# Kernel tuning notes

Measured on AMD Instinct MI355X. Metric: run time of the kernel, lower is better.

Reference implementation:

```python
import jax, jax.numpy as jnp
import numpy as np

MARGIN = 2.0


def setup_inputs() -> dict:
    key = jax.random.key(0)
    k1, k2 = jax.random.split(key)
    B, D, NUM_CLASSES = 8192, 128, 100
    features = jax.random.normal(k1, (B, D), dtype=jnp.float32)
    labels = jax.random.randint(k2, (B,), 0, NUM_CLASSES, dtype=jnp.int64)
    return {"features": features, "labels": labels}


def reference(features, labels):
    # Vectorized form of the O(B^2) nested-loop contrastive loss.
    B = features.shape[0]
    sq = jnp.sum(features * features, axis=-1)                      # [B]
    # squared pairwise L2 distances via the gram matrix
    d2 = sq[:, None] + sq[None, :] - 2.0 * (features @ features.T)  # [B, B]
    d2 = jnp.maximum(d2, 0.0)

    off_diag = ~jnp.eye(B, dtype=bool)
    same = labels[:, None] == labels[None, :]
    pos_mask = same & off_diag
    neg_mask = (~same) & off_diag

    # positive pairs contribute squared distance
    pos_loss = jnp.sum(jnp.where(pos_mask, d2, 0.0))

    # negative pairs contribute clamp(margin - dist, 0)^2; guard sqrt(0) grads
    d = jnp.sqrt(jnp.where(neg_mask, d2, 1.0))
    hinge = jnp.maximum(MARGIN - d, 0.0)
    neg_loss = jnp.sum(jnp.where(neg_mask, hinge * hinge, 0.0))

    pos_count = jnp.sum(pos_mask)
    total_pairs = jnp.asarray(B * (B - 1), dtype=d2.dtype)
    loss = pos_loss + neg_loss
    # original divides only when positive_pairs > 0
    return jnp.where(pos_count > 0, loss / total_pairs, loss)
```

## Files before the change

kernel.cpp:

```cpp
#include <hip/hip_runtime.h>
#include <hip/hip_bf16.h>


#define BN 8192
#define DD 128
#define NTILES 64
#define NBLOCKS (NTILES * (NTILES + 1) / 2)

typedef __attribute__((ext_vector_type(8))) short bf16x8;
typedef __attribute__((ext_vector_type(4))) float f32x4;

__global__ __launch_bounds__(256) void prep_kernel(const float* __restrict__ f,
        const int* __restrict__ labels, short* __restrict__ fbp,
        float2* __restrict__ meta) {
    const int tid = threadIdx.x;
    const int wave = tid >> 6, lane = tid & 63;
    const int p = blockIdx.x * 4 + wave;
    const int l15 = lane & 15, quad = lane >> 4;
    const int row = p * 16 + l15;

    float s = 0.f;
#pragma unroll
    for (int ks = 0; ks < 4; ks++) {
        const float* src = f + (size_t)row * DD + ks * 32 + quad * 8;
        float4 a = *(const float4*)src;
        float4 b = *(const float4*)(src + 4);
        unsigned short u[8];
        float rv[8] = {a.x, a.y, a.z, a.w, b.x, b.y, b.z, b.w};
#pragma unroll
        for (int j = 0; j < 8; j++) {
            __hip_bfloat16 h = __float2bfloat16(rv[j]);
            u[j] = *(unsigned short*)&h;
            float r = __bfloat162float(h);
            s = fmaf(r, r, s);
        }
        bf16x8 pack;
#pragma unroll
        for (int j = 0; j < 8; j++) pack[j] = (short)u[j];
        *(bf16x8*)(fbp + ((size_t)(p * 4 + ks) * 64 + lane) * 8) = pack;
    }
    s += __shfl_xor(s, 16, 64);
    s += __shfl_xor(s, 32, 64);
    if (quad == 0) meta[row] = make_float2(s, (float)labels[row]);
}

__global__ __launch_bounds__(256) void pair_kernel(
        const short* __restrict__ fbp, const float2* __restrict__ meta,
        float2* __restrict__ partial) {
    const int t = blockIdx.x;
    int by = (int)((sqrtf(8.f * (float)t + 1.f) - 1.f) * 0.5f);
    while ((by + 1) * (by + 2) / 2 <= t) by++;
    while (by * (by + 1) / 2 > t) by--;
    const int bx = t - by * (by + 1) / 2;
    const bool diag = (bx == by);

    const int tid = threadIdx.x;
    const int wave = tid >> 6, lane = tid & 63;
    const int wx = wave & 1, wy = wave >> 1;
    const int i0 = bx * 128 + wy * 64;
    const int j0 = by * 128 + wx * 64;
    const int ip = i0 >> 4, jp = j0 >> 4;
    const int l15 = lane & 15, quad = lane >> 4;

    float pos = 0.f, neg = 0.f;

    if (!(diag && wx < wy)) {
        float2 mj[4];
#pragma unroll
        for (int ni = 0; ni < 4; ni++) mj[ni] = meta[j0 + ni * 16 + l15];
        float2 mi[4][4];
#pragma unroll
        for (int m = 0; m < 4; m++)
#pragma unroll
            for (int r = 0; r < 4; r++) mi[m][r] = meta[i0 + m * 16 + quad * 4 + r];

        f32x4 acc4[4][4];
#pragma unroll
        for (int a = 0; a < 4; a++)
#pragma unroll
            for (int b = 0; b < 4; b++) acc4[a][b] = (f32x4){0.f, 0.f, 0.f, 0.f};

#pragma unroll
        for (int ks = 0; ks < 4; ks++) {
            bf16x8 af[4], bg[4];
#pragma unroll
            for (int tt = 0; tt < 4; tt++)
                af[tt] = *(const bf16x8*)(fbp +
                    ((size_t)((ip + tt) * 4 + ks) * 64 + lane) * 8);
#pragma unroll
            for (int tt = 0; tt < 4; tt++)
                bg[tt] = *(const bf16x8*)(fbp +
                    ((size_t)((jp + tt) * 4 + ks) * 64 + lane) * 8);
#pragma unroll
            for (int m = 0; m < 4; m++)
#pragma unroll
                for (int n = 0; n < 4; n++)
                    acc4[m][n] = __builtin_amdgcn_mfma_f32_16x16x32_bf16(
                        af[m], bg[n], acc4[m][n], 0, 0, 0);
        }

        const bool strict = diag && (wx == wy);
#pragma unroll
        for (int m = 0; m < 4; m++)
#pragma unroll
            for (int n = 0; n < 4; n++)
#pragma unroll
                for (int r = 0; r < 4; r++) {
                    int il = m * 16 + quad * 4 + r;
                    int jl = n * 16 + l15;
                    bool valid = !strict || (il < jl);
                    float d2 = fmaxf(mi[m][r].x + mj[n].x - 2.f * acc4[m][n][r], 0.f);
                    if (valid) {
                        if (mi[m][r].y == mj[n].y) pos += d2;
                        else if (d2 < 4.0f) {
                            float h = 2.0f - sqrtf(d2);
                            neg += h * h;
                        }
                    }
                }
    }

#pragma unroll
    for (int off = 32; off > 0; off >>= 1) {
        pos += __shfl_down(pos, off, 64);
        neg += __shfl_down(neg, off, 64);
    }
    __shared__ float red[2][4];
    if (lane == 0) { red[0][wave] = pos; red[1][wave] = neg; }
    __syncthreads();
    if (tid == 0)
        partial[t] = make_float2(red[0][0] + red[0][1] + red[0][2] + red[0][3],
                                 red[1][0] + red[1][1] + red[1][2] + red[1][3]);
}

__global__ __launch_bounds__(256) void reduce_kernel(
        const float2* __restrict__ partial, float* __restrict__ out) {
    const int tid = threadIdx.x;
    float p = 0.f, n = 0.f;
    for (int i = tid; i < NBLOCKS; i += 256) {
        float2 v = partial[i];
        p += v.x; n += v.y;
    }
#pragma unroll
    for (int off = 32; off > 0; off >>= 1) {
        p += __shfl_down(p, off, 64);
        n += __shfl_down(n, off, 64);
    }
    __shared__ float red[2][4];
    int lane = tid & 63, w = tid >> 6;
    if (lane == 0) { red[0][w] = p; red[1][w] = n; }
    __syncthreads();
    if (tid == 0) {
        float total = 2.0f * (red[0][0] + red[0][1] + red[0][2] + red[0][3] +
                              red[1][0] + red[1][1] + red[1][2] + red[1][3]);
        out[0] = total / 67100672.0f;
    }
}

extern "C" void kernel_launch(void* const* d_in, const int* in_sizes, int n_in,
                              void* d_out, int out_size, void* d_ws, size_t ws_size,
                              hipStream_t stream) {
    const float* f = (const float*)d_in[0];
    const int* labels = (const int*)d_in[1];
    float* out = (float*)d_out;

    short* fbp = (short*)d_ws;
    float2* meta = (float2*)((char*)d_ws + (size_t)BN * DD * sizeof(short));
    float2* partial = meta + BN;

    prep_kernel<<<BN / 64, 256, 0, stream>>>(f, labels, fbp, meta);
    pair_kernel<<<NBLOCKS, 256, 0, stream>>>(fbp, meta, partial);
    reduce_kernel<<<1, 256, 0, stream>>>(partial, out);
}
```

Measured before the change: 89.76 us.

## Coalesce prep loads via LDS transpose and double-buffer MFMA operand loads

The prep kernel now has each block handle 16 rows. It reads them with fully coalesced row-contiguous float4 loads, converts to bf16 into padded shared memory, and then writes the MFMA-packed layout from LDS. The old version used strided per-lane reads. The grid grows to BN/16 blocks. In the pair kernel, the k-step loop is manually software-pipelined with two register buffers so global loads for the next k-slice are issued before the current MFMAs. This hides load latency at the cost of extra VGPRs.

New measurement: 88.19 us. Within noise of the previous version (-1.8%).

```diff
diff --git a/kernel.cpp b/kernel.cpp
--- a/kernel.cpp
+++ b/kernel.cpp
@@ -6,6 +6,7 @@
 #define DD 128
 #define NTILES 64
 #define NBLOCKS (NTILES * (NTILES + 1) / 2)
+#define LS 136
 
 typedef __attribute__((ext_vector_type(8))) short bf16x8;
 typedef __attribute__((ext_vector_type(4))) float f32x4;
@@ -14,34 +15,32 @@
         const int* __restrict__ labels, short* __restrict__ fbp,
         float2* __restrict__ meta) {
     const int tid = threadIdx.x;
-    const int wave = tid >> 6, lane = tid & 63;
-    const int p = blockIdx.x * 4 + wave;
-    const int l15 = lane & 15, quad = lane >> 4;
-    const int row = p * 16 + l15;
+    const int p = blockIdx.x;
+    __shared__ unsigned short ls[16][LS];
 
+    const int r = tid >> 4;
+    const int c = (tid & 15) * 8;
+    const float* src = f + ((size_t)p * 16 + r) * DD + c;
+    float4 a = *(const float4*)src;
+    float4 b = *(const float4*)(src + 4);
+    float rv[8] = {a.x, a.y, a.z, a.w, b.x, b.y, b.z, b.w};
     float s = 0.f;
 #pragma unroll
-    for (int ks = 0; ks < 4; ks++) {
-        const float* src = f + (size_t)row * DD + ks * 32 + quad * 8;
-        float4 a = *(const float4*)src;
-        float4 b = *(const float4*)(src + 4);
-        unsigned short u[8];
-        float rv[8] = {a.x, a.y, a.z, a.w, b.x, b.y, b.z, b.w};
+    for (int j = 0; j < 8; j++) {
+        __hip_bfloat16 h = __float2bfloat16(rv[j]);
+        ls[r][c + j] = *(unsigned short*)&h;
+        float rr = __bfloat162float(h);
+        s = fmaf(rr, rr, s);
+    }
 #pragma unroll
-        for (int j = 0; j < 8; j++) {
-            __hip_bfloat16 h = __float2bfloat16(rv[j]);
-            u[j] = *(unsigned short*)&h;
-            float r = __bfloat162float(h);
-            s = fmaf(r, r, s);
-        }
-        bf16x8 pack;
-#pragma unroll
-        for (int j = 0; j < 8; j++) pack[j] = (short)u[j];
-        *(bf16x8*)(fbp + ((size_t)(p * 4 + ks) * 64 + lane) * 8) = pack;
-    }
-    s += __shfl_xor(s, 16, 64);
-    s += __shfl_xor(s, 32, 64);
-    if (quad == 0) meta[row] = make_float2(s, (float)labels[row]);
+    for (int off = 8; off > 0; off >>= 1) s += __shfl_down(s, off, 16);
+    if ((tid & 15) == 0) meta[p * 16 + r] = make_float2(s, (float)labels[p * 16 + r]);
+    __syncthreads();
+
+    const int w = tid >> 6, lane = tid & 63;
+    const int l15 = lane & 15, quad = lane >> 4;
+    bf16x8 pack = *(const bf16x8*)&ls[l15][w * 32 + quad * 8];
+    *(bf16x8*)(fbp + ((size_t)(p * 4 + w) * 64 + lane) * 8) = pack;
 }
 
 __global__ __launch_bounds__(256) void pair_kernel(
@@ -80,9 +79,7 @@
 #pragma unroll
             for (int b = 0; b < 4; b++) acc4[a][b] = (f32x4){0.f, 0.f, 0.f, 0.f};
 
-#pragma unroll
-        for (int ks = 0; ks < 4; ks++) {
-            bf16x8 af[4], bg[4];
+        auto loadf = [&](int ks, bf16x8* af, bf16x8* bg) {
 #pragma unroll
             for (int tt = 0; tt < 4; tt++)
                 af[tt] = *(const bf16x8*)(fbp +
@@ -91,13 +88,25 @@
             for (int tt = 0; tt < 4; tt++)
                 bg[tt] = *(const bf16x8*)(fbp +
                     ((size_t)((jp + tt) * 4 + ks) * 64 + lane) * 8);
+        };
+        auto mfma16 = [&](bf16x8* af, bf16x8* bg) {
 #pragma unroll
             for (int m = 0; m < 4; m++)
 #pragma unroll
                 for (int n = 0; n < 4; n++)
                     acc4[m][n] = __builtin_amdgcn_mfma_f32_16x16x32_bf16(
                         af[m], bg[n], acc4[m][n], 0, 0, 0);
-        }
+        };
+
+        bf16x8 a0[4], b0[4], a1[4], b1[4];
+        loadf(0, a0, b0);
+        loadf(1, a1, b1);
+        mfma16(a0, b0);
+        loadf(2, a0, b0);
+        mfma16(a1, b1);
+        loadf(3, a1, b1);
+        mfma16(a0, b0);
+        mfma16(a1, b1);
 
         const bool strict = diag && (wx == wy);
 #pragma unroll
@@ -168,7 +177,7 @@
     float2* meta = (float2*)((char*)d_ws + (size_t)BN * DD * sizeof(short));
     float2* partial = meta + BN;
 
-    prep_kernel<<<BN / 64, 256, 0, stream>>>(f, labels, fbp, meta);
+    prep_kernel<<<BN / 16, 256, 0, stream>>>(f, labels, fbp, meta);
     pair_kernel<<<NBLOCKS, 256, 0, stream>>>(fbp, meta, partial);
     reduce_kernel<<<1, 256, 0, stream>>>(partial, out);
 }
```
